# Optimization experiments

Measured on AMD Instinct MI355X. Metric: run time of the kernel, lower is better.

The kernel has to match this reference:

```python
import jax, jax.numpy as jnp
import numpy as np

B, N, G, M = 16, 2048, 128, 32
DM, NL, DI, DS, DTR, DC = 384, 12, 768, 16, 24, 4
EPS = 1e-5


def _silu(x):
    return x * jax.nn.sigmoid(x)


def _ln(x, w, b):
    mu = x.mean(-1, keepdims=True)
    v = ((x - mu) ** 2).mean(-1, keepdims=True)
    return (x - mu) * jax.lax.rsqrt(v + EPS) * w + b


def _bn_eval(x, g, b):
    # eval-mode BatchNorm1d (running mean=0, var=1)
    return x * (g * jax.lax.rsqrt(jnp.float32(1.0) + EPS)) + b


def _fps(pts):
    # farthest point sampling, pts [N,3] -> [G] indices (starts at index 0)
    n = pts.shape[0]
    def body(carry, _):
        dmin, i = carry
        dd = jnp.sum((pts - pts[i]) ** 2, -1)
        dmin = jnp.minimum(dmin, dd)
        return (dmin, jnp.argmax(dmin).astype(jnp.int32)), i
    init = (jnp.full((n,), 1e10, pts.dtype), jnp.array(0, jnp.int32))
    (_, _), idx = jax.lax.scan(body, init, None, length=G)
    return idx


def _group(xyz):
    cidx = jax.vmap(_fps)(xyz)                                   # [B,G]
    center = jnp.take_along_axis(xyz, cidx[..., None], axis=1)    # [B,G,3]
    d2 = jnp.sum((center[:, :, None, :] - xyz[:, None, :, :]) ** 2, -1)  # [B,G,N]
    _, nidx = jax.lax.top_k(-d2, M)                               # [B,G,M]
    nb = jax.vmap(lambda p, i: p[i])(xyz, nidx)                   # [B,G,M,3]
    return nb - center[:, :, None, :], center


def _mixer(x, in_w, cw, cb, xp_w, dt_w, dt_b, A_log, Dp, out_w):
    b, L, _ = x.shape
    xz = jnp.einsum('bld,ed->ble', x, in_w)                       # [B,L,2*DI]
    xin, z = xz[..., :DI], xz[..., DI:]
    xpad = jnp.pad(xin, ((0, 0), (DC - 1, 0), (0, 0)))            # causal depthwise conv
    xin = _silu(sum(xpad[:, k:k + L, :] * cw[:, k] for k in range(DC)) + cb)
    dbl = jnp.einsum('bld,ed->ble', xin, xp_w)                    # [B,L,DTR+2*DS]
    dt = jax.nn.softplus(jnp.einsum('blr,dr->bld', dbl[..., :DTR], dt_w) + dt_b)
    Bm, Cm = dbl[..., DTR:DTR + DS], dbl[..., DTR + DS:]
    A = -jnp.exp(A_log)                                           # [DI,DS]
    dA = jnp.exp(dt[..., None] * A)                               # [B,L,DI,DS]
    dBx = (dt * xin)[..., None] * Bm[:, :, None, :]               # [B,L,DI,DS]
    def step(h, inp):
        dA_t, dBx_t, C_t = inp
        h = dA_t * h + dBx_t
        return h, jnp.einsum('bds,bs->bd', h, C_t)
    h0 = jnp.zeros((b, DI, DS), x.dtype)
    _, ys = jax.lax.scan(step, h0, (jnp.swapaxes(dA, 0, 1), jnp.swapaxes(dBx, 0, 1), jnp.swapaxes(Cm, 0, 1)))
    y = jnp.swapaxes(ys, 0, 1) + Dp * xin
    return jnp.einsum('bld,ed->ble', y * _silu(z), out_w)


def forward_fn(xyz, e1w1, e1b1, bn1g, bn1b, e1w2, e1b2, e2w1, e2b1, bn2g, bn2b,
               e2w2, e2b2, pw1, pb1, pw2, pb2, in_w, conv_w, conv_b, xp_w,
               dt_w, dt_b, A_log, Dp, out_w, lnw, lnb, fnw, fnb):
    nb, center = _group(xyz)
    # Encoder (1x1 convs == pointwise linears) over [B*G, M, 3]
    x = nb.reshape(B * G, M, 3)
    f = jax.nn.relu(_bn_eval(x @ e1w1.T + e1b1, bn1g, bn1b))
    f = f @ e1w2.T + e1b2                                         # [BG,M,256]
    fg = f.max(axis=1, keepdims=True)
    f = jnp.concatenate([jnp.broadcast_to(fg, (B * G, M, 256)), f], -1)
    f = jax.nn.relu(_bn_eval(f @ e2w1.T + e2b1, bn2g, bn2b))
    f = f @ e2w2.T + e2b2                                         # [BG,M,DM]
    tokens = f.max(axis=1).reshape(B, G, DM)
    pos = jax.nn.gelu(center @ pw1.T + pb1) @ pw2.T + pb2
    h = tokens + pos
    residual = None
    for i in range(NL):
        residual = h + residual if residual is not None else h
        h = _mixer(_ln(residual, lnw[i], lnb[i]), in_w[i], conv_w[i], conv_b[i],
                   xp_w[i], dt_w[i], dt_b[i], A_log[i], Dp[i], out_w[i])
    return _ln(h + residual, fnw, fnb)


def setup_inputs() -> dict:
    ks = jax.random.split(jax.random.key(0), 16)
    r = lambda i, s, sc=0.02: jax.random.normal(ks[i], s, jnp.float32) * sc
    dt_init = float(np.log(np.expm1(0.01)))
    return {
        'xyz': jax.random.normal(ks[0], (B, N, 3), jnp.float32),
        'e1w1': r(1, (128, 3), 0.3), 'e1b1': jnp.zeros(128),
        'bn1g': jnp.ones(128), 'bn1b': jnp.zeros(128),
        'e1w2': r(2, (256, 128), 0.05), 'e1b2': jnp.zeros(256),
        'e2w1': r(3, (512, 512), 0.03), 'e2b1': jnp.zeros(512),
        'bn2g': jnp.ones(512), 'bn2b': jnp.zeros(512),
        'e2w2': r(4, (DM, 512), 0.03), 'e2b2': jnp.zeros(DM),
        'pw1': r(5, (128, 3), 0.3), 'pb1': jnp.zeros(128),
        'pw2': r(6, (DM, 128), 0.05), 'pb2': jnp.zeros(DM),
        'in_w': r(7, (NL, 2 * DI, DM)),
        'conv_w': r(8, (NL, DI, DC), 0.2), 'conv_b': jnp.zeros((NL, DI)),
        'xp_w': r(9, (NL, DTR + 2 * DS, DI)),
        'dt_w': r(10, (NL, DI, DTR), 0.1),
        'dt_b': jnp.full((NL, DI), dt_init, jnp.float32),
        'A_log': jnp.log(jnp.broadcast_to(jnp.arange(1, DS + 1, dtype=jnp.float32), (NL, DI, DS)) + 0.0),
        'Dp': jnp.ones((NL, DI)),
        'out_w': r(11, (NL, DM, DI)),
        'lnw': jnp.ones((NL, DM)), 'lnb': jnp.zeros((NL, DM)),
        'fnw': jnp.ones(DM), 'fnb': jnp.zeros(DM),
    }


def reference(xyz, e1w1, e1b1, bn1g, bn1b, e1w2, e1b2, e2w1, e2b1, bn2g, bn2b,
              e2w2, e2b2, pw1, pb1, pw2, pb2, in_w, conv_w, conv_b, xp_w,
              dt_w, dt_b, A_log, Dp, out_w, lnw, lnb, fnw, fnb):
    return forward_fn(xyz, e1w1, e1b1, bn1g, bn1b, e1w2, e1b2, e2w1, e2b1,
                      bn2g, bn2b, e2w2, e2b2, pw1, pb1, pw2, pb2, in_w, conv_w,
                      conv_b, xp_w, dt_w, dt_b, A_log, Dp, out_w, lnw, lnb, fnw, fnb)
```

## Files before the change

### kernel.cpp

```cpp
#include <hip/hip_runtime.h>
#include <hip/hip_bf16.h>
#include <math.h>

#define PN   2048
#define PB   16
#define PG   128
#define PM   32
#define PDM  384
#define PDI  768
#define ROWS 2048

typedef unsigned short ushort_t;
typedef unsigned int uint_t;
typedef unsigned long long ull_t;
typedef __attribute__((ext_vector_type(8))) short bf8;
typedef __attribute__((ext_vector_type(4))) float f4;

__device__ __forceinline__ ushort_t f2bf(float x) {
  unsigned int u = __float_as_uint(x);
  unsigned int r = (u + 0x7FFFu + ((u >> 16) & 1u)) >> 16;
  return (ushort_t)r;
}
__device__ __forceinline__ float bf2f(ushort_t u) {
  return __uint_as_float(((unsigned)u) << 16);
}
__device__ __forceinline__ ull_t umax64(ull_t a, ull_t b) { return a > b ? a : b; }
__device__ __forceinline__ ull_t umin64(ull_t a, ull_t b) { return a < b ? a : b; }

__device__ __forceinline__ float rowsum16(float v) {
  v += __int_as_float(__builtin_amdgcn_update_dpp(0, __float_as_int(v), 0x121, 0xF, 0xF, false));
  v += __int_as_float(__builtin_amdgcn_update_dpp(0, __float_as_int(v), 0x122, 0xF, 0xF, false));
  v += __int_as_float(__builtin_amdgcn_update_dpp(0, __float_as_int(v), 0x124, 0xF, 0xF, false));
  v += __int_as_float(__builtin_amdgcn_update_dpp(0, __float_as_int(v), 0x128, 0xF, 0xF, false));
  return v;
}

#define GL2L(gp, lp) __builtin_amdgcn_global_load_lds((const __attribute__((address_space(1))) void*)(gp), (__attribute__((address_space(3))) void*)(lp), 16, 0, 0)

#define CV_O1 32768
#define CV_O2 294912
#define CV_O3 491520
#define CV_O4 7569408
#define CV_TOT 11108352
#define DTWT_TOT (12*768*24)
#define XPWT_TOT (12*192*64*4)
#define PREP_TOT (CV_TOT + DTWT_TOT + XPWT_TOT)
__global__ __launch_bounds__(256) void prep_kernel(
    const float* __restrict__ e1w2, const float* __restrict__ e2w1,
    const float* __restrict__ e2w2, const float* __restrict__ in_w,
    const float* __restrict__ out_w, const float* __restrict__ dt_w,
    const float* __restrict__ xp_w,
    ushort_t* __restrict__ wb, float* __restrict__ dtwT,
    float* __restrict__ xpwT) {
  int i = blockIdx.x*256 + threadIdx.x;
  if (i >= PREP_TOT) return;
  if (i < CV_TOT) {
    const float* s; int off;
    if      (i < CV_O1) { s = e1w2;  off = 0; }
    else if (i < CV_O2) { s = e2w1;  off = CV_O1; }
    else if (i < CV_O3) { s = e2w2;  off = CV_O2; }
    else if (i < CV_O4) { s = in_w;  off = CV_O3; }
    else                { s = out_w; off = CV_O4; }
    wb[i] = f2bf(s[i - off]);
  } else if (i < CV_TOT + DTWT_TOT) {
    int j = i - CV_TOT;
    int layer = j / (768*24);
    int rem = j - layer*768*24;
    int d = rem / 24, r = rem - d*24;
    dtwT[layer*24*768 + r*768 + d] = dt_w[j];
  } else {
    int j = i - CV_TOT - DTWT_TOT;
    int layer = j / 49152;
    int rem = j - layer*49152;
    int r4 = rem >> 8;
    int rem2 = rem & 255;
    int e = rem2 >> 2, jj = rem2 & 3;
    xpwT[j] = (e < 56) ? xp_w[(size_t)layer*56*768 + (size_t)e*768 + r4*4 + jj] : 0.f;
  }
}

__global__ __launch_bounds__(256) void fps_kernel(const float* __restrict__ xyz,
                                                  int* __restrict__ cidx) {
  const int b = blockIdx.x;
  const int tid = threadIdx.x;
  const int wave = tid >> 6, lane = tid & 63;
  __shared__ float pts[PN*3];
  __shared__ ull_t kws[2][4];
  const float* base = xyz + (size_t)b * PN * 3;
  for (int t = tid; t < PN*3; t += 256) pts[t] = base[t];
  __syncthreads();
  float px[8], py[8], pz[8], dmin[8];
  #pragma unroll
  for (int j = 0; j < 8; ++j) {
    int idx = j*256 + tid;
    px[j] = pts[idx*3+0]; py[j] = pts[idx*3+1]; pz[j] = pts[idx*3+2];
    dmin[j] = 1e10f;
  }
  int cur = 0;
  for (int g = 0; g < PG; ++g) {
    if (tid == 0) cidx[b*PG + g] = cur;
    const float cx = pts[cur*3+0], cy = pts[cur*3+1], cz = pts[cur*3+2];
    ull_t k[8];
    #pragma unroll
    for (int j = 0; j < 8; ++j) {
      float dx = __fsub_rn(px[j], cx);
      float dy = __fsub_rn(py[j], cy);
      float dz = __fsub_rn(pz[j], cz);
      float dd = __fadd_rn(__fadd_rn(__fmul_rn(dx,dx), __fmul_rn(dy,dy)), __fmul_rn(dz,dz));
      float dm = fminf(dmin[j], dd);
      dmin[j] = dm;
      k[j] = ((ull_t)__float_as_uint(dm) << 32) | (unsigned)(~(unsigned)(j*256 + tid));
    }
    ull_t a0 = umax64(k[0], k[1]), a1 = umax64(k[2], k[3]);
    ull_t a2 = umax64(k[4], k[5]), a3 = umax64(k[6], k[7]);
    ull_t K = umax64(umax64(a0, a1), umax64(a2, a3));
    #pragma unroll
    for (int off = 1; off < 64; off <<= 1)
      K = umax64(K, (ull_t)__shfl_xor((unsigned long long)K, off));
    const int par = g & 1;
    if (lane == 0) kws[par][wave] = K;
    __syncthreads();
    ull_t K0 = umax64(umax64(kws[par][0], kws[par][1]), umax64(kws[par][2], kws[par][3]));
    cur = (int)(~(unsigned)(K0 & 0xFFFFFFFFull));
  }
}

__global__ __launch_bounds__(64) void knn_kernel(const float* __restrict__ xyz,
                                                 const int* __restrict__ cidx,
                                                 float* __restrict__ nbx,
                                                 float* __restrict__ centerb) {
  const int bg = blockIdx.x;
  const int b = bg >> 7;
  const int lane = threadIdx.x;
  const float* base = xyz + (size_t)b * PN * 3;
  const int ci = cidx[bg];
  const float cx = base[ci*3+0], cy = base[ci*3+1], cz = base[ci*3+2];
  if (lane == 0) { centerb[bg*3+0]=cx; centerb[bg*3+1]=cy; centerb[bg*3+2]=cz; }
  float d2[32];
  #pragma unroll
  for (int j = 0; j < 32; ++j) {
    int idx = j*64 + lane;
    float dx = __fsub_rn(cx, base[idx*3+0]);
    float dy = __fsub_rn(cy, base[idx*3+1]);
    float dz = __fsub_rn(cz, base[idx*3+2]);
    d2[j] = __fadd_rn(__fadd_rn(__fmul_rn(dx,dx), __fmul_rn(dy,dy)), __fmul_rn(dz,dz));
  }
  for (int m = 0; m < PM; ++m) {
    ull_t t[16];
    #pragma unroll
    for (int j = 0; j < 16; ++j) {
      ull_t e0 = ((ull_t)__float_as_uint(d2[j])     << 32) | (unsigned)(j*64 + lane);
      ull_t e1 = ((ull_t)__float_as_uint(d2[j+16])  << 32) | (unsigned)((j+16)*64 + lane);
      t[j] = umin64(e0, e1);
    }
    #pragma unroll
    for (int s = 8; s >= 1; s >>= 1)
      #pragma unroll
      for (int j = 0; j < 16; ++j) if (j < s) t[j] = umin64(t[j], t[j+s]);
    ull_t K = t[0];
    #pragma unroll
    for (int off = 1; off < 64; off <<= 1)
      K = umin64(K, (ull_t)__shfl_xor((unsigned long long)K, off));
    const int k = __builtin_amdgcn_readfirstlane((int)(unsigned)(K & 0xFFFFFFFFull));
    const int jwin = k >> 6, owner = k & 63;
    #pragma unroll
    for (int j = 0; j < 32; ++j)
      if (j == jwin && lane == owner) d2[j] = 1e38f;
    if (lane == 0) {
      nbx[(bg*PM + m)*3 + 0] = base[k*3+0] - cx;
      nbx[(bg*PM + m)*3 + 1] = base[k*3+1] - cy;
      nbx[(bg*PM + m)*3 + 2] = base[k*3+2] - cz;
    }
  }
}

__global__ __launch_bounds__(256) void embed1_kernel(
    const float* __restrict__ nbx,
    const float* __restrict__ e1w1, const float* __restrict__ e1b1,
    const float* __restrict__ bn1g, const float* __restrict__ bn1b,
    const ushort_t* __restrict__ e1w2b, const float* __restrict__ e1b2,
    ushort_t* __restrict__ f2b, ushort_t* __restrict__ fgb) {
  const int bg = blockIdx.x;
  const int tid = threadIdx.x;
  const int wid = tid >> 6, lane = tid & 63;
  const int q = lane >> 4, r16 = lane & 15;
  __shared__ float xs[PM*3];
  __shared__ __align__(16) ushort_t Af[4*2*64*8];
  __shared__ __align__(16) ushort_t Bs[16*64*8];
  if (tid < PM*3) xs[tid] = nbx[bg*PM*3 + tid];
  __syncthreads();
  const float bns = rsqrtf(1.0f + 1e-5f);
  #pragma unroll
  for (int it = 0; it < 16; ++it) {
    int id = tid + it*256;
    int m = id >> 7, c = id & 127;
    float v = xs[m*3+0]*e1w1[c*3+0] + xs[m*3+1]*e1w1[c*3+1] + xs[m*3+2]*e1w1[c*3+2] + e1b1[c];
    v = fmaxf(v * (bn1g[c]*bns) + bn1b[c], 0.0f);
    int kc = c >> 5, cc = c & 31, qq = cc >> 3, j = cc & 7;
    int t = m >> 4, r = m & 15;
    Af[((kc*2 + t)*64 + qq*16 + r)*8 + j] = f2bf(v);
  }
  f4 acc[2][4];
  #pragma unroll
  for (int t = 0; t < 2; ++t)
    #pragma unroll
    for (int jj = 0; jj < 4; ++jj) { f4 z = {0.f,0.f,0.f,0.f}; acc[t][jj] = z; }
  for (int kc = 0; kc < 4; ++kc) {
    #pragma unroll
    for (int u = wid; u < 16; u += 4)
      GL2L(e1w2b + (size_t)(u*16 + r16)*128 + kc*32 + q*8, Bs + u*512);
    __syncthreads();
    bf8 a0 = *(const bf8*)(Af + ((size_t)((kc*2+0)*64 + lane))*8);
    bf8 a1 = *(const bf8*)(Af + ((size_t)((kc*2+1)*64 + lane))*8);
    #pragma unroll
    for (int jj = 0; jj < 4; ++jj) {
      bf8 bv = *(const bf8*)(Bs + ((size_t)((wid*4+jj)*64 + lane))*8);
      acc[0][jj] = __builtin_amdgcn_mfma_f32_16x16x32_bf16(a0, bv, acc[0][jj], 0, 0, 0);
      acc[1][jj] = __builtin_amdgcn_mfma_f32_16x16x32_bf16(a1, bv, acc[1][jj], 0, 0, 0);
    }
    __syncthreads();
  }
  #pragma unroll
  for (int jj = 0; jj < 4; ++jj) {
    const int n = (wid*4+jj)*16 + r16;
    const float bias = e1b2[n];
    float v0[4], v1[4];
    float cm = -1e30f;
    #pragma unroll
    for (int rr = 0; rr < 4; ++rr) {
      v0[rr] = acc[0][jj][rr] + bias;
      v1[rr] = acc[1][jj][rr] + bias;
      cm = fmaxf(cm, fmaxf(v0[rr], v1[rr]));
    }
    cm = fmaxf(cm, __shfl_xor(cm, 16));
    cm = fmaxf(cm, __shfl_xor(cm, 32));
    #pragma unroll
    for (int rr = 0; rr < 4; ++rr) {
      f2b[((size_t)bg*32 + q*4 + rr)*256 + n]      = f2bf(v0[rr]);
      f2b[((size_t)bg*32 + 16 + q*4 + rr)*256 + n] = f2bf(v1[rr]);
    }
    if (lane < 16) fgb[(size_t)bg*256 + n] = f2bf(cm);
  }
}

template<int MT, int NT, int EPI>
__global__ __launch_bounds__(256) void mfma_gemm(
    const ushort_t* __restrict__ A, int lda,
    const ushort_t* __restrict__ W, int ldw,
    float* __restrict__ Cf, ushort_t* __restrict__ Cb, int ldc, int K,
    const float* __restrict__ p0, const float* __restrict__ p1,
    const float* __restrict__ p2, const float* __restrict__ p3) {
  static_assert(EPI != 2 || MT == 4, "groupmax needs MT=4");
  constexpr int AT = 2*MT, BT = 2*NT;
  __shared__ __align__(16) ushort_t As[2*AT*512];
  __shared__ __align__(16) ushort_t Bs[2*BT*512];
  const int tid = threadIdx.x;
  const int wid = tid >> 6, lane = tid & 63;
  const int wr = wid >> 1, wc = wid & 1;
  const int q = lane >> 4, r16 = lane & 15;
  const int m0 = blockIdx.y * (32*MT);
  const int n0 = blockIdx.x * (32*NT);
  f4 acc[MT][NT];
  #pragma unroll
  for (int i = 0; i < MT; ++i)
    #pragma unroll
    for (int j = 0; j < NT; ++j) { f4 z = {0.f,0.f,0.f,0.f}; acc[i][j] = z; }

  for (int k0 = 0; k0 < K; k0 += 64) {
    #pragma unroll
    for (int c = 0; c < 2; ++c) {
      const int kk = k0 + c*32 + q*8;
      #pragma unroll
      for (int t = wid; t < AT; t += 4)
        GL2L(A + (size_t)(m0 + t*16 + r16)*lda + kk, As + (c*AT + t)*512);
      #pragma unroll
      for (int t = wid; t < BT; t += 4)
        GL2L(W + (size_t)(n0 + t*16 + r16)*ldw + kk, Bs + (c*BT + t)*512);
    }
    __syncthreads();
    #pragma unroll
    for (int c = 0; c < 2; ++c) {
      bf8 af[MT], bfr[NT];
      #pragma unroll
      for (int i = 0; i < MT; ++i)
        af[i] = *(const bf8*)(As + ((size_t)(c*AT + wr*MT+i)*64 + lane)*8);
      #pragma unroll
      for (int j = 0; j < NT; ++j)
        bfr[j] = *(const bf8*)(Bs + ((size_t)(c*BT + wc*NT+j)*64 + lane)*8);
      #pragma unroll
      for (int i = 0; i < MT; ++i)
        #pragma unroll
        for (int j = 0; j < NT; ++j)
          acc[i][j] = __builtin_amdgcn_mfma_f32_16x16x32_bf16(af[i], bfr[j], acc[i][j], 0, 0, 0);
    }
    __syncthreads();
  }

  if constexpr (EPI == 0) {
    #pragma unroll
    for (int i = 0; i < MT; ++i) {
      const int row = m0 + (wr*MT+i)*16 + q*4;
      #pragma unroll
      for (int j = 0; j < NT; ++j) {
        const int col = n0 + (wc*NT+j)*16 + r16;
        #pragma unroll
        for (int r = 0; r < 4; ++r)
          Cf[(size_t)(row+r)*ldc + col] = acc[i][j][r];
      }
    }
  } else if constexpr (EPI == 1) {
    const float bns = rsqrtf(1.0f + 1e-5f);
    #pragma unroll
    for (int j = 0; j < NT; ++j) {
      const int col = n0 + (wc*NT+j)*16 + r16;
      const float b1 = p0[col], sg = p1[col]*bns, b2 = p2[col];
      #pragma unroll
      for (int i = 0; i < MT; ++i) {
        const int row = m0 + (wr*MT+i)*16 + q*4;
        #pragma unroll
        for (int r = 0; r < 4; ++r) {
          const int grp = (row + r) >> 5;
          float v = fmaxf(fmaf(acc[i][j][r] + b1 + p3[(size_t)grp*512 + col], sg, b2), 0.0f);
          Cb[(size_t)(row+r)*ldc + col] = f2bf(v);
        }
      }
    }
  } else if constexpr (EPI == 3) {
    #pragma unroll
    for (int i = 0; i < MT; ++i) {
      const int row = m0 + (wr*MT+i)*16 + q*4;
      #pragma unroll
      for (int j = 0; j < NT; ++j) {
        const int col = n0 + (wc*NT+j)*16 + r16;
        #pragma unroll
        for (int r = 0; r < 4; ++r)
          Cb[(size_t)(row+r)*ldc + col] = f2bf(acc[i][j][r]);
      }
    }
  } else {
    #pragma unroll
    for (int j = 0; j < NT; ++j) {
      const int col = n0 + (wc*NT+j)*16 + r16;
      float tm[4];
      #pragma unroll
      for (int i = 0; i < 4; ++i) {
        float t = fmaxf(fmaxf(acc[i][j][0], acc[i][j][1]), fmaxf(acc[i][j][2], acc[i][j][3]));
        t = fmaxf(t, __shfl_xor(t, 16));
        t = fmaxf(t, __shfl_xor(t, 32));
        tm[i] = t;
      }
      const float bias = p0[col];
      if (lane < 16) {
        const int g0 = (m0 >> 5) + wr*2;
        Cf[(size_t)g0*ldc + col]     = fmaxf(tm[0], tm[1]) + bias;
        Cf[(size_t)(g0+1)*ldc + col] = fmaxf(tm[2], tm[3]) + bias;
      }
    }
  }
}

__global__ __launch_bounds__(128) void prenorm0_kernel(
    const float* __restrict__ h, const float* __restrict__ centerb,
    const float* __restrict__ pw1, const float* __restrict__ pb1,
    const float* __restrict__ pw2, const float* __restrict__ pb2,
    float* __restrict__ res,
    const float* __restrict__ w, const float* __restrict__ bb,
    ushort_t* __restrict__ xo) {
  const int row = blockIdx.x;
  const int tid = threadIdx.x;
  __shared__ float t1[128];
  __shared__ float s1[2], s2[2];
  const float cx = centerb[row*3+0], cy = centerb[row*3+1], cz = centerb[row*3+2];
  {
    const int c = tid;
    float v = cx*pw1[c*3+0] + cy*pw1[c*3+1] + cz*pw1[c*3+2] + pb1[c];
    float u = 0.7978845608028654f * (v + 0.044715f*v*v*v);
    t1[c] = 0.5f*v*(1.0f + tanhf(u));
  }
  __syncthreads();
  float v[3];
  #pragma unroll
  for (int i = 0; i < 3; ++i) {
    int j = tid + i*128;
    float acc = pb2[j];
    const float4* wp = (const float4*)(pw2 + (size_t)j*128);
    const float4* a = (const float4*)t1;
    for (int k4 = 0; k4 < 32; ++k4) {
      float4 wv = wp[k4], av = a[k4];
      acc = fmaf(av.x, wv.x, fmaf(av.y, wv.y, fmaf(av.z, wv.z, fmaf(av.w, wv.w, acc))));
    }
    float r = h[(size_t)row*PDM + j] + acc;
    res[(size_t)row*PDM + j] = r;
    v[i] = r;
  }
  float ss = v[0] + v[1] + v[2];
  #pragma unroll
  for (int off = 1; off < 64; off <<= 1) ss += __shfl_xor(ss, off);
  if ((tid & 63) == 0) s1[tid>>6] = ss;
  __syncthreads();
  const float mu = (s1[0] + s1[1]) * (1.0f/384.0f);
  float qq = 0.f;
  #pragma unroll
  for (int i = 0; i < 3; ++i) { float d = v[i] - mu; qq += d*d; }
  #pragma unroll
  for (int off = 1; off < 64; off <<= 1) qq += __shfl_xor(qq, off);
  if ((tid & 63) == 0) s2[tid>>6] = qq;
  __syncthreads();
  const float rs = rsqrtf((s2[0] + s2[1]) * (1.0f/384.0f) + 1e-5f);
  #pragma unroll
  for (int i = 0; i < 3; ++i) {
    int j = tid + i*128;
    xo[(size_t)row*PDM + j] = f2bf((v[i] - mu) * rs * w[j] + bb[j]);
  }
}

__global__ __launch_bounds__(128) void prenorm_kernel(
    const float* __restrict__ h, float* __restrict__ res,
    const float* __restrict__ w, const float* __restrict__ bb,
    ushort_t* __restrict__ xo) {
  const int row = blockIdx.x;
  const int tid = threadIdx.x;
  __shared__ float s1[2], s2[2];
  float v[3];
  #pragma unroll
  for (int i = 0; i < 3; ++i) {
    int j = tid + i*128;
    float r = h[(size_t)row*PDM + j] + res[(size_t)row*PDM + j];
    res[(size_t)row*PDM + j] = r;
    v[i] = r;
  }
  float ss = v[0] + v[1] + v[2];
  #pragma unroll
  for (int off = 1; off < 64; off <<= 1) ss += __shfl_xor(ss, off);
  if ((tid & 63) == 0) s1[tid>>6] = ss;
  __syncthreads();
  const float mu = (s1[0] + s1[1]) * (1.0f/384.0f);
  float qq = 0.f;
  #pragma unroll
  for (int i = 0; i < 3; ++i) { float d = v[i] - mu; qq += d*d; }
  #pragma unroll
  for (int off = 1; off < 64; off <<= 1) qq += __shfl_xor(qq, off);
  if ((tid & 63) == 0) s2[tid>>6] = qq;
  __syncthreads();
  const float rs = rsqrtf((s2[0] + s2[1]) * (1.0f/384.0f) + 1e-5f);
  #pragma unroll
  for (int i = 0; i < 3; ++i) {
    int j = tid + i*128;
    xo[(size_t)row*PDM + j] = f2bf((v[i] - mu) * rs * w[j] + bb[j]);
  }
}

__global__ __launch_bounds__(128) void final_kernel(
    const float* __restrict__ h, const float* __restrict__ res,
    const float* __restrict__ w, const float* __restrict__ bb,
    float* __restrict__ out) {
  const int row = blockIdx.x;
  const int tid = threadIdx.x;
  __shared__ float s1[2], s2[2];
  float v[3];
  #pragma unroll
  for (int i = 0; i < 3; ++i) {
    int j = tid + i*128;
    v[i] = h[(size_t)row*PDM + j] + res[(size_t)row*PDM + j];
  }
  float ss = v[0] + v[1] + v[2];
  #pragma unroll
  for (int off = 1; off < 64; off <<= 1) ss += __shfl_xor(ss, off);
  if ((tid & 63) == 0) s1[tid>>6] = ss;
  __syncthreads();
  const float mu = (s1[0] + s1[1]) * (1.0f/384.0f);
  float qq = 0.f;
  #pragma unroll
  for (int i = 0; i < 3; ++i) { float d = v[i] - mu; qq += d*d; }
  #pragma unroll
  for (int off = 1; off < 64; off <<= 1) qq += __shfl_xor(qq, off);
  if ((tid & 63) == 0) s2[tid>>6] = qq;
  __syncthreads();
  const float rs = rsqrtf((s2[0] + s2[1]) * (1.0f/384.0f) + 1e-5f);
  #pragma unroll
  for (int i = 0; i < 3; ++i) {
    int j = tid + i*128;
    out[(size_t)row*PDM + j] = (v[i] - mu) * rs * w[j] + bb[j];
  }
}

__global__ __launch_bounds__(256) void cxd_kernel(
    const ushort_t* __restrict__ xzb,
    const float* __restrict__ cw, const float* __restrict__ cb,
    const float* __restrict__ xpwT,
    ushort_t* __restrict__ xinb, float* __restrict__ dbl) {
  const int row = blockIdx.x;
  const int tid = threadIdx.x;
  const int wid = tid >> 6, lane = tid & 63;
  const int l = row & 127;
  const int bb = row - l;
  __shared__ float xin_s[PDI];
  __shared__ float part[4][64];
  #pragma unroll
  for (int i = 0; i < 3; ++i) {
    const int d = tid + i*256;
    float acc = cb[d];
    #pragma unroll
    for (int k = 0; k < 4; ++k) {
      int ll = l + k - 3;
      if (ll >= 0) acc = fmaf(bf2f(xzb[(size_t)(bb+ll)*1536 + d]), cw[d*4+k], acc);
    }
    float s = 1.0f / (1.0f + __expf(-acc));
    float v = acc * s;
    xin_s[d] = v;
    xinb[(size_t)row*PDI + d] = f2bf(v);
  }
  __syncthreads();
  {
    const float4* wp = (const float4*)xpwT;
    float a = 0.f;
    const int base_r4 = wid*48;
    for (int t = 0; t < 48; ++t) {
      const int r4 = base_r4 + t;
      float4 w4 = wp[r4*64 + lane];
      float4 x4 = *(const float4*)&xin_s[r4*4];
      a = fmaf(x4.x, w4.x, fmaf(x4.y, w4.y, fmaf(x4.z, w4.z, fmaf(x4.w, w4.w, a))));
    }
    part[wid][lane] = a;
  }
  __syncthreads();
  if (tid < 64) {
    float v = part[0][tid] + part[1][tid] + part[2][tid] + part[3][tid];
    if (tid < 56) dbl[(size_t)row*56 + tid] = v;
  }
}

__global__ __launch_bounds__(256) void scan_kernel(
    const ushort_t* __restrict__ xzb,
    const ushort_t* __restrict__ xinb,
    const float* __restrict__ dbl,
    const float* __restrict__ dtwT, const float* __restrict__ dtbias,
    const float* __restrict__ alog, const float* __restrict__ dp,
    ushort_t* __restrict__ yb) {
  const int d0 = blockIdx.x * 16;
  const int b  = blockIdx.y;
  const int tid = threadIdx.x;
  __shared__ float dbl_s[128*56];
  __shared__ float dts[128*16];
  __shared__ float dtw_s[24*16];
  __shared__ ushort_t xins[128*16];
  __shared__ ushort_t zs[128*16];
  __shared__ ushort_t ys[128*16];
  {
    const float4* src = (const float4*)(dbl + (size_t)b*128*56);
    float4* dst = (float4*)dbl_s;
    for (int i = tid; i < 1792; i += 256) dst[i] = src[i];
  }
  for (int i = tid; i < 24*16; i += 256) {
    int r = i >> 4, c = i & 15;
    dtw_s[i] = dtwT[r*768 + d0 + c];
  }
  for (int i = tid; i < 1024; i += 256) {
    int l = i >> 3, c2 = (i & 7)*2;
    *(uint_t*)&xins[l*16 + c2] = *(const uint_t*)(xinb + ((size_t)(b*128 + l))*768 + d0 + c2);
    *(uint_t*)&zs[l*16 + c2]   = *(const uint_t*)(xzb + ((size_t)(b*128 + l))*1536 + 768 + d0 + c2);
  }
  __syncthreads();
  for (int i = tid; i < 2048; i += 256) {
    int l = i >> 4, c = i & 15;
    float acc = dtbias[d0 + c];
    #pragma unroll
    for (int r = 0; r < 24; ++r) acc = fmaf(dbl_s[l*56 + r], dtw_s[r*16 + c], acc);
    dts[i] = log1pf(expf(-fabsf(acc))) + fmaxf(acc, 0.0f);
  }
  __syncthreads();
  const int s = tid & 15, dl = tid >> 4;
  const int d = d0 + dl;
  const float A = -expf(alog[d*16 + s]);
  const float Dv = dp[d];
  float h = 0.f;
  #pragma unroll 4
  for (int l = 0; l < 128; ++l) {
    float dtv = dts[l*16 + dl];
    float xv  = bf2f(xins[l*16 + dl]);
    float Bv  = dbl_s[l*56 + 24 + s];
    float Cv  = dbl_s[l*56 + 40 + s];
    float dA = __expf(dtv * A);
    h = fmaf(dA, h, dtv * xv * Bv);
    float p = rowsum16(h * Cv);
    if (s == 0) {
      float z = bf2f(zs[l*16 + dl]);
      float sg = 1.0f / (1.0f + __expf(-z));
      ys[l*16 + dl] = f2bf(fmaf(Dv, xv, p) * z * sg);
    }
  }
  __syncthreads();
  for (int i = tid; i < 1024; i += 256) {
    int l = i >> 3, c2 = (i & 7)*2;
    *(uint_t*)(yb + ((size_t)(b*128 + l))*768 + d0 + c2) = *(const uint_t*)&ys[l*16 + c2];
  }
}

extern "C" void kernel_launch(void* const* d_in, const int* in_sizes, int n_in,
                              void* d_out, int out_size, void* d_ws, size_t ws_size,
                              hipStream_t stream) {
  const float* xyz    = (const float*)d_in[0];
  const float* e1w1   = (const float*)d_in[1];
  const float* e1b1   = (const float*)d_in[2];
  const float* bn1g   = (const float*)d_in[3];
  const float* bn1b   = (const float*)d_in[4];
  const float* e1w2   = (const float*)d_in[5];
  const float* e1b2   = (const float*)d_in[6];
  const float* e2w1   = (const float*)d_in[7];
  const float* e2b1   = (const float*)d_in[8];
  const float* bn2g   = (const float*)d_in[9];
  const float* bn2b   = (const float*)d_in[10];
  const float* e2w2   = (const float*)d_in[11];
  const float* e2b2   = (const float*)d_in[12];
  const float* pw1    = (const float*)d_in[13];
  const float* pb1    = (const float*)d_in[14];
  const float* pw2    = (const float*)d_in[15];
  const float* pb2    = (const float*)d_in[16];
  const float* in_w   = (const float*)d_in[17];
  const float* conv_w = (const float*)d_in[18];
  const float* conv_b = (const float*)d_in[19];
  const float* xp_w   = (const float*)d_in[20];
  const float* dt_w   = (const float*)d_in[21];
  const float* dt_b   = (const float*)d_in[22];
  const float* A_log  = (const float*)d_in[23];
  const float* Dp     = (const float*)d_in[24];
  const float* out_w  = (const float*)d_in[25];
  const float* lnw    = (const float*)d_in[26];
  const float* lnb    = (const float*)d_in[27];
  const float* fnw    = (const float*)d_in[28];
  const float* fnb    = (const float*)d_in[29];

  char* ws = (char*)d_ws;
  size_t off = 0;
  auto alloc = [&](size_t bytes) { void* p = ws + off; off += (bytes + 255) & ~(size_t)255; return p; };
  int*      cidx    = (int*)     alloc(PB*PG*4);
  float*    centerb = (float*)   alloc(ROWS*3*4);
  float*    nbx     = (float*)   alloc(ROWS*PM*3*4);
  ushort_t* f2b     = (ushort_t*)alloc((size_t)ROWS*PM*256*2);
  ushort_t* fgb     = (ushort_t*)alloc((size_t)ROWS*256*2);
  float*    gbuf    = (float*)   alloc((size_t)ROWS*512*4);
  ushort_t* f3      = (ushort_t*)alloc((size_t)ROWS*PM*512*2);
  float*    hbuf    = (float*)   alloc((size_t)ROWS*PDM*4);
  float*    resid   = (float*)   alloc((size_t)ROWS*PDM*4);
  ushort_t* xlnb    = (ushort_t*)alloc((size_t)ROWS*PDM*2);
  ushort_t* xzb     = (ushort_t*)alloc((size_t)ROWS*1536*2);
  ushort_t* xinb    = (ushort_t*)alloc((size_t)ROWS*PDI*2);
  float*    dbl     = (float*)   alloc((size_t)ROWS*56*4);
  ushort_t* ybufb   = (ushort_t*)alloc((size_t)ROWS*PDI*2);
  ushort_t* wb      = (ushort_t*)alloc((size_t)CV_TOT*2);
  float*    dtwT    = (float*)   alloc((size_t)DTWT_TOT*4);
  float*    xpwT    = (float*)   alloc((size_t)XPWT_TOT*4);

  ushort_t* e1w2b  = wb;
  ushort_t* e2w1b  = wb + CV_O1;
  ushort_t* e2w2b  = wb + CV_O2;
  ushort_t* in_wb  = wb + CV_O3;
  ushort_t* out_wb = wb + CV_O4;

  prep_kernel<<<(PREP_TOT+255)/256, 256, 0, stream>>>(
      e1w2, e2w1, e2w2, in_w, out_w, dt_w, xp_w, wb, dtwT, xpwT);

  fps_kernel<<<PB, 256, 0, stream>>>(xyz, cidx);
  knn_kernel<<<ROWS, 64, 0, stream>>>(xyz, cidx, nbx, centerb);
  embed1_kernel<<<ROWS, 256, 0, stream>>>(nbx, e1w1, e1b1, bn1g, bn1b, e1w2b, e1b2, f2b, fgb);

  mfma_gemm<2,4,0><<<dim3(4, 32), 256, 0, stream>>>(
      fgb, 256, e2w1b, 512, gbuf, nullptr, 512, 256, nullptr, nullptr, nullptr, nullptr);
  mfma_gemm<4,4,1><<<dim3(4, 512), 256, 0, stream>>>(
      f2b, 256, e2w1b + 256, 512, nullptr, f3, 512, 256, e2b1, bn2g, bn2b, gbuf);
  mfma_gemm<4,4,2><<<dim3(3, 512), 256, 0, stream>>>(
      f3, 512, e2w2b, 512, hbuf, nullptr, PDM, 512, e2b2, nullptr, nullptr, nullptr);

  prenorm0_kernel<<<ROWS, 128, 0, stream>>>(hbuf, centerb, pw1, pb1, pw2, pb2,
                                            resid, lnw, lnb, xlnb);

  for (int i = 0; i < 12; ++i) {
    mfma_gemm<2,4,3><<<dim3(12, 32), 256, 0, stream>>>(
        xlnb, PDM, in_wb + (size_t)i*1536*384, PDM, nullptr, xzb, 1536, PDM,
        nullptr, nullptr, nullptr, nullptr);
    cxd_kernel<<<ROWS, 256, 0, stream>>>(
        xzb, conv_w + (size_t)i*768*4, conv_b + (size_t)i*768,
        xpwT + (size_t)i*49152, xinb, dbl);
    scan_kernel<<<dim3(48, PB), 256, 0, stream>>>(
        xzb, xinb, dbl, dtwT + (size_t)i*24*768, dt_b + (size_t)i*768,
        A_log + (size_t)i*768*16, Dp + (size_t)i*768, ybufb);
    mfma_gemm<2,2,0><<<dim3(6, 32), 256, 0, stream>>>(
        ybufb, PDI, out_wb + (size_t)i*384*768, PDI, hbuf, nullptr, PDM, PDI,
        nullptr, nullptr, nullptr, nullptr);
    if (i < 11)
      prenorm_kernel<<<ROWS, 128, 0, stream>>>(hbuf, resid, lnw + (i+1)*384, lnb + (i+1)*384, xlnb);
    else
      final_kernel<<<ROWS, 128, 0, stream>>>(hbuf, resid, fnw, fnb, (float*)d_out);
  }
}
```

Before: 1.543 ms.

## Fuse layernorm into in-projection GEMM and residual add into out-projection epilogue

Adds a new in-projection kernel that computes per-row LayerNorm statistics from the fp32 residual, normalizes and packs bf16 A-fragments into shared memory, then runs the MFMA GEMM against the in_w weights. The out-projection GEMM gains an epilogue that accumulates directly into the residual buffer, removing the per-layer prenorm kernel and the intermediate xln and hbuf round trips. Each in-projection block recomputes LN statistics for its 64 rows (12 column blocks redundantly), and variance now uses the E[x^2]-mu^2 form, which is slightly less numerically stable.

New measurement: 1.665 ms. 1.08x slower.

```diff
diff --git a/kernel.cpp b/kernel.cpp
--- a/kernel.cpp
+++ b/kernel.cpp
@@ -337,6 +337,20 @@
           Cb[(size_t)(row+r)*ldc + col] = f2bf(acc[i][j][r]);
       }
     }
+  } else if constexpr (EPI == 4) {
+    #pragma unroll
+    for (int i = 0; i < MT; ++i) {
+      const int row = m0 + (wr*MT+i)*16 + q*4;
+      #pragma unroll
+      for (int j = 0; j < NT; ++j) {
+        const int col = n0 + (wc*NT+j)*16 + r16;
+        #pragma unroll
+        for (int r = 0; r < 4; ++r) {
+          float t = acc[i][j][r] + Cf[(size_t)(row+r)*ldc + col];
+          Cf[(size_t)(row+r)*ldc + col] = t;
+        }
+      }
+    }
   } else {
     #pragma unroll
     for (int j = 0; j < NT; ++j) {
@@ -359,17 +373,120 @@
   }
 }
 
+__global__ __launch_bounds__(256) void ln_inproj_kernel(
+    const float* __restrict__ resid,
+    const float* __restrict__ lw, const float* __restrict__ lb,
+    const ushort_t* __restrict__ W,
+    ushort_t* __restrict__ xzb) {
+  __shared__ __align__(16) ushort_t Afr[12*4*64*8];
+  __shared__ __align__(16) ushort_t Bs[2*8*512];
+  __shared__ float wS[384], bS[384];
+  __shared__ float partS[64][4], partQ[64][4];
+  __shared__ float muS[64], rsS[64];
+  const int tid = threadIdx.x;
+  const int wid = tid >> 6, lane = tid & 63;
+  const int wr = wid >> 1, wc = wid & 1;
+  const int q = lane >> 4, r16 = lane & 15;
+  const int m0 = blockIdx.y * 64;
+  const int n0 = blockIdx.x * 128;
+  for (int i = tid; i < 384; i += 256) { wS[i] = lw[i]; bS[i] = lb[i]; }
+  const int row = tid >> 2, part = tid & 3;
+  {
+    const float4* rp = (const float4*)(resid + (size_t)(m0 + row)*384 + part*96);
+    float s = 0.f, qq2 = 0.f;
+    #pragma unroll
+    for (int k = 0; k < 24; ++k) {
+      float4 v = rp[k];
+      s += v.x + v.y + v.z + v.w;
+      qq2 = fmaf(v.x, v.x, fmaf(v.y, v.y, fmaf(v.z, v.z, fmaf(v.w, v.w, qq2))));
+    }
+    partS[row][part] = s; partQ[row][part] = qq2;
+  }
+  __syncthreads();
+  if (tid < 64) {
+    float s = partS[tid][0] + partS[tid][1] + partS[tid][2] + partS[tid][3];
+    float qq2 = partQ[tid][0] + partQ[tid][1] + partQ[tid][2] + partQ[tid][3];
+    float mu = s * (1.0f/384.0f);
+    float var = qq2 * (1.0f/384.0f) - mu*mu;
+    muS[tid] = mu;
+    rsS[tid] = rsqrtf(var + 1e-5f);
+  }
+  __syncthreads();
+  {
+    const float mu = muS[row], rs = rsS[row];
+    const int t = row >> 4, r15 = row & 15;
+    const float* rp = resid + (size_t)(m0 + row)*384;
+    #pragma unroll
+    for (int k = 0; k < 12; ++k) {
+      const int c0 = part*96 + k*8;
+      float4 a = *(const float4*)(rp + c0);
+      float4 b4 = *(const float4*)(rp + c0 + 4);
+      bf8 pk;
+      pk[0] = (short)f2bf((a.x - mu)*rs*wS[c0+0] + bS[c0+0]);
+      pk[1] = (short)f2bf((a.y - mu)*rs*wS[c0+1] + bS[c0+1]);
+      pk[2] = (short)f2bf((a.z - mu)*rs*wS[c0+2] + bS[c0+2]);
+      pk[3] = (short)f2bf((a.w - mu)*rs*wS[c0+3] + bS[c0+3]);
+      pk[4] = (short)f2bf((b4.x - mu)*rs*wS[c0+4] + bS[c0+4]);
+      pk[5] = (short)f2bf((b4.y - mu)*rs*wS[c0+5] + bS[c0+5]);
+      pk[6] = (short)f2bf((b4.z - mu)*rs*wS[c0+6] + bS[c0+6]);
+      pk[7] = (short)f2bf((b4.w - mu)*rs*wS[c0+7] + bS[c0+7]);
+      const int kc = c0 >> 5, qq = (c0 & 31) >> 3;
+      *(bf8*)(Afr + ((size_t)((kc*4 + t)*64 + qq*16 + r15))*8) = pk;
+    }
+  }
+  __syncthreads();
+  f4 acc[2][4];
+  #pragma unroll
+  for (int i = 0; i < 2; ++i)
+    #pragma unroll
+    for (int j = 0; j < 4; ++j) { f4 z = {0.f,0.f,0.f,0.f}; acc[i][j] = z; }
+  for (int k0 = 0; k0 < 6; ++k0) {
+    #pragma unroll
+    for (int c = 0; c < 2; ++c) {
+      #pragma unroll
+      for (int t = wid; t < 8; t += 4)
+        GL2L(W + (size_t)(n0 + t*16 + r16)*384 + k0*64 + c*32 + q*8, Bs + (c*8 + t)*512);
+    }
+    __syncthreads();
+    #pragma unroll
+    for (int c = 0; c < 2; ++c) {
+      const int kc = k0*2 + c;
+      bf8 af[2], bfr[4];
+      #pragma unroll
+      for (int i = 0; i < 2; ++i)
+        af[i] = *(const bf8*)(Afr + ((size_t)((kc*4 + wr*2 + i)*64 + lane))*8);
+      #pragma unroll
+      for (int j = 0; j < 4; ++j)
+        bfr[j] = *(const bf8*)(Bs + ((size_t)((c*8 + wc*4 + j)*64 + lane))*8);
+      #pragma unroll
+      for (int i = 0; i < 2; ++i)
+        #pragma unroll
+        for (int j = 0; j < 4; ++j)
+          acc[i][j] = __builtin_amdgcn_mfma_f32_16x16x32_bf16(af[i], bfr[j], acc[i][j], 0, 0, 0);
+    }
+    __syncthreads();
+  }
+  #pragma unroll
+  for (int i = 0; i < 2; ++i) {
+    const int r0 = m0 + (wr*2 + i)*16 + q*4;
+    #pragma unroll
+    for (int j = 0; j < 4; ++j) {
+      const int col = n0 + (wc*4 + j)*16 + r16;
+      #pragma unroll
+      for (int r = 0; r < 4; ++r)
+        xzb[(size_t)(r0 + r)*1536 + col] = f2bf(acc[i][j][r]);
+    }
+  }
+}
+
 __global__ __launch_bounds__(128) void prenorm0_kernel(
     const float* __restrict__ h, const float* __restrict__ centerb,
     const float* __restrict__ pw1, const float* __restrict__ pb1,
     const float* __restrict__ pw2, const float* __restrict__ pb2,
-    float* __restrict__ res,
-    const float* __restrict__ w, const float* __restrict__ bb,
-    ushort_t* __restrict__ xo) {
+    float* __restrict__ res) {
   const int row = blockIdx.x;
   const int tid = threadIdx.x;
   __shared__ float t1[128];
-  __shared__ float s1[2], s2[2];
   const float cx = centerb[row*3+0], cy = centerb[row*3+1], cz = centerb[row*3+2];
   {
     const int c = tid;
@@ -378,7 +495,6 @@
     t1[c] = 0.5f*v*(1.0f + tanhf(u));
   }
   __syncthreads();
-  float v[3];
   #pragma unroll
   for (int i = 0; i < 3; ++i) {
     int j = tid + i*128;
@@ -389,69 +505,12 @@
       float4 wv = wp[k4], av = a[k4];
       acc = fmaf(av.x, wv.x, fmaf(av.y, wv.y, fmaf(av.z, wv.z, fmaf(av.w, wv.w, acc))));
     }
-    float r = h[(size_t)row*PDM + j] + acc;
-    res[(size_t)row*PDM + j] = r;
-    v[i] = r;
-  }
-  float ss = v[0] + v[1] + v[2];
-  #pragma unroll
-  for (int off = 1; off < 64; off <<= 1) ss += __shfl_xor(ss, off);
-  if ((tid & 63) == 0) s1[tid>>6] = ss;
-  __syncthreads();
-  const float mu = (s1[0] + s1[1]) * (1.0f/384.0f);
-  float qq = 0.f;
-  #pragma unroll
-  for (int i = 0; i < 3; ++i) { float d = v[i] - mu; qq += d*d; }
-  #pragma unroll
-  for (int off = 1; off < 64; off <<= 1) qq += __shfl_xor(qq, off);
-  if ((tid & 63) == 0) s2[tid>>6] = qq;
-  __syncthreads();
-  const float rs = rsqrtf((s2[0] + s2[1]) * (1.0f/384.0f) + 1e-5f);
-  #pragma unroll
-  for (int i = 0; i < 3; ++i) {
-    int j = tid + i*128;
-    xo[(size_t)row*PDM + j] = f2bf((v[i] - mu) * rs * w[j] + bb[j]);
-  }
-}
-
-__global__ __launch_bounds__(128) void prenorm_kernel(
-    const float* __restrict__ h, float* __restrict__ res,
-    const float* __restrict__ w, const float* __restrict__ bb,
-    ushort_t* __restrict__ xo) {
-  const int row = blockIdx.x;
-  const int tid = threadIdx.x;
-  __shared__ float s1[2], s2[2];
-  float v[3];
-  #pragma unroll
-  for (int i = 0; i < 3; ++i) {
-    int j = tid + i*128;
-    float r = h[(size_t)row*PDM + j] + res[(size_t)row*PDM + j];
-    res[(size_t)row*PDM + j] = r;
-    v[i] = r;
-  }
-  float ss = v[0] + v[1] + v[2];
-  #pragma unroll
-  for (int off = 1; off < 64; off <<= 1) ss += __shfl_xor(ss, off);
-  if ((tid & 63) == 0) s1[tid>>6] = ss;
-  __syncthreads();
-  const float mu = (s1[0] + s1[1]) * (1.0f/384.0f);
-  float qq = 0.f;
-  #pragma unroll
-  for (int i = 0; i < 3; ++i) { float d = v[i] - mu; qq += d*d; }
-  #pragma unroll
-  for (int off = 1; off < 64; off <<= 1) qq += __shfl_xor(qq, off);
-  if ((tid & 63) == 0) s2[tid>>6] = qq;
-  __syncthreads();
-  const float rs = rsqrtf((s2[0] + s2[1]) * (1.0f/384.0f) + 1e-5f);
-  #pragma unroll
-  for (int i = 0; i < 3; ++i) {
-    int j = tid + i*128;
-    xo[(size_t)row*PDM + j] = f2bf((v[i] - mu) * rs * w[j] + bb[j]);
+    res[(size_t)row*PDM + j] = h[(size_t)row*PDM + j] + acc;
   }
 }
 
 __global__ __launch_bounds__(128) void final_kernel(
-    const float* __restrict__ h, const float* __restrict__ res,
+    const float* __restrict__ res,
     const float* __restrict__ w, const float* __restrict__ bb,
     float* __restrict__ out) {
   const int row = blockIdx.x;
@@ -459,10 +518,7 @@
   __shared__ float s1[2], s2[2];
   float v[3];
   #pragma unroll
-  for (int i = 0; i < 3; ++i) {
-    int j = tid + i*128;
-    v[i] = h[(size_t)row*PDM + j] + res[(size_t)row*PDM + j];
-  }
+  for (int i = 0; i < 3; ++i) v[i] = res[(size_t)row*PDM + tid + i*128];
   float ss = v[0] + v[1] + v[2];
   #pragma unroll
   for (int off = 1; off < 64; off <<= 1) ss += __shfl_xor(ss, off);
@@ -642,7 +698,6 @@
   ushort_t* f3      = (ushort_t*)alloc((size_t)ROWS*PM*512*2);
   float*    hbuf    = (float*)   alloc((size_t)ROWS*PDM*4);
   float*    resid   = (float*)   alloc((size_t)ROWS*PDM*4);
-  ushort_t* xlnb    = (ushort_t*)alloc((size_t)ROWS*PDM*2);
   ushort_t* xzb     = (ushort_t*)alloc((size_t)ROWS*1536*2);
   ushort_t* xinb    = (ushort_t*)alloc((size_t)ROWS*PDI*2);
   float*    dbl     = (float*)   alloc((size_t)ROWS*56*4);
@@ -671,25 +726,21 @@
   mfma_gemm<4,4,2><<<dim3(3, 512), 256, 0, stream>>>(
       f3, 512, e2w2b, 512, hbuf, nullptr, PDM, 512, e2b2, nullptr, nullptr, nullptr);
 
-  prenorm0_kernel<<<ROWS, 128, 0, stream>>>(hbuf, centerb, pw1, pb1, pw2, pb2,
-                                            resid, lnw, lnb, xlnb);
+  prenorm0_kernel<<<ROWS, 128, 0, stream>>>(hbuf, centerb, pw1, pb1, pw2, pb2, resid);
 
   for (int i = 0; i < 12; ++i) {
-    mfma_gemm<2,4,3><<<dim3(12, 32), 256, 0, stream>>>(
-        xlnb, PDM, in_wb + (size_t)i*1536*384, PDM, nullptr, xzb, 1536, PDM,
-        nullptr, nullptr, nullptr, nullptr);
+    ln_inproj_kernel<<<dim3(12, 32), 256, 0, stream>>>(
+        resid, lnw + i*384, lnb + i*384, in_wb + (size_t)i*1536*384, xzb);
     cxd_kernel<<<ROWS, 256, 0, stream>>>(
         xzb, conv_w + (size_t)i*768*4, conv_b + (size_t)i*768,
         xpwT + (size_t)i*49152, xinb, dbl);
     scan_kernel<<<dim3(48, PB), 256, 0, stream>>>(
         xzb, xinb, dbl, dtwT + (size_t)i*24*768, dt_b + (size_t)i*768,
         A_log + (size_t)i*768*16, Dp + (size_t)i*768, ybufb);
-    mfma_gemm<2,2,0><<<dim3(6, 32), 256, 0, stream>>>(
-        ybufb, PDI, out_wb + (size_t)i*384*768, PDI, hbuf, nullptr, PDM, PDI,
+    mfma_gemm<2,2,4><<<dim3(6, 32), 256, 0, stream>>>(
+        ybufb, PDI, out_wb + (size_t)i*384*768, PDI, resid, nullptr, PDM, PDI,
         nullptr, nullptr, nullptr, nullptr);
-    if (i < 11)
-      prenorm_kernel<<<ROWS, 128, 0, stream>>>(hbuf, resid, lnw + (i+1)*384, lnb + (i+1)*384, xlnb);
-    else
-      final_kernel<<<ROWS, 128, 0, stream>>>(hbuf, resid, fnw, fnb, (float*)d_out);
-  }
-}
+  }
+
+  final_kernel<<<ROWS, 128, 0, stream>>>(resid, fnw, fnb, (float*)d_out);
+}
```
